# Kernel tuning notes

Measured on AMD Instinct MI355X. Metric: run time of the kernel, lower is better.

Reference implementation:

```python
import jax, jax.numpy as jnp
import numpy as np

TOP_K = 8
DILATION = 2
KERNEL = 7
W_POS = 1.0
W_NEG = 0.1
EPS = 1e-8  # torch F.cosine_similarity eps


def unfold(x, k, d):
    # nn.Unfold(kernel_size=k, padding=(k//2)*d, dilation=d) -> [B, C, k*k, H, W]
    B, C, H, W = x.shape
    p = (k // 2) * d
    xp = jnp.pad(x, ((0, 0), (0, 0), (p, p), (p, p)))
    patches = [xp[:, :, i * d:i * d + H, j * d:j * d + W]
               for i in range(k) for j in range(k)]
    return jnp.stack(patches, axis=2)


def setup_inputs() -> dict:
    key = jax.random.key(0)
    k1, k2, k3, k4 = jax.random.split(key, 4)
    return {
        "logits_trg": jax.random.normal(k1, (2, 19, 128, 128), dtype=jnp.float32),
        "logits_ema": jax.random.normal(k2, (2, 19, 64, 64), dtype=jnp.float32),
        "x_ema": jax.random.normal(k3, (2, 64, 32, 32), dtype=jnp.float32),
        "mix_masks": jax.random.uniform(k4, (2, 1, 128, 128), dtype=jnp.float32),
    }


def reference(logits_trg, logits_ema, x_ema, mix_masks):
    B, C, H, W = logits_trg.shape
    # ignore_mask_trg = F.interpolate(1 - mix_masks, (H,W), 'nearest') > 0.5 (already at (H,W))
    ignore = (1.0 - mix_masks) > 0.5  # [B,1,H,W] bool

    # logits_ema bilinear upsample to (H,W) (align_corners=False == half-pixel)
    logits_ema_up = jax.image.resize(logits_ema, (B, C, H, W), method='bilinear')
    unf_logits = unfold(logits_ema_up, KERNEL, DILATION)  # [B,C,K,H,W], K=k^2

    # get_sim_feat: nearest upsample (integer factor == torch 'nearest') then cosine sim
    f = H // x_ema.shape[2]
    feats = jnp.repeat(jnp.repeat(x_ema, f, axis=2), f, axis=3)  # [B,Cf,H,W]
    unf_feats = unfold(feats, KERNEL, DILATION)                  # [B,Cf,K,H,W]
    dot = jnp.einsum('bckhw,bchw->bkhw', unf_feats, feats)
    n_u = jnp.maximum(jnp.sqrt(jnp.sum(unf_feats * unf_feats, axis=1)), EPS)  # [B,K,H,W]
    n_c = jnp.maximum(jnp.sqrt(jnp.sum(feats * feats, axis=1)), EPS)          # [B,H,W]
    sim_feat = dot / (n_u * n_c[:, None])  # [B,K,H,W]

    # top-k over kernel window (largest top_k+1, smallest top_k)
    sim_t = jnp.moveaxis(sim_feat, 1, -1)             # [B,H,W,K]
    vmax, imax = jax.lax.top_k(sim_t, TOP_K + 1)
    vneg, imin = jax.lax.top_k(-sim_t, TOP_K)
    vmin = -vneg

    def weighted_agg(vals, idx):
        # vals/idx: [B,H,W,t] -> weighted sum of gathered logits over window -> [B,C,H,W]
        idx = jnp.moveaxis(idx, -1, 1)    # [B,t,H,W]
        vals = jnp.moveaxis(vals, -1, 1)  # [B,t,H,W]
        t = idx.shape[1]
        idxb = jnp.broadcast_to(idx[:, None], (B, C, t, H, W))
        g = jnp.take_along_axis(unf_logits, idxb, axis=2)  # [B,C,t,H,W]
        return jnp.sum(vals[:, None] * g, axis=2)

    pl_pos = jax.nn.softmax(weighted_agg(vmax, imax), axis=1)
    pl_neg = jax.nn.softmax(weighted_agg(vmin, imin), axis=1)

    def bce_with_logits(x, z):
        # -(z*log(sig(x)) + (1-z)*log(1-sig(x))) = (1-z)*x - log_sigmoid(x)
        return (1.0 - z) * x - jax.nn.log_sigmoid(x)

    m = ignore.astype(logits_trg.dtype)  # [B,1,H,W]
    denom = jnp.sum(m) * C               # mask repeated across C classes
    loss_pos = jnp.sum(bce_with_logits(logits_trg, pl_pos) * m) / denom
    loss_neg = jnp.sum(-bce_with_logits(logits_trg, pl_neg) * m) / denom
    return jnp.stack([loss_pos * W_POS, loss_neg * W_NEG])
```

## Files before the change

### kernel.cpp

```cpp
#include <hip/hip_runtime.h>
#include <math.h>

#define NB 2
#define NC 19
#define NH 128
#define NW 128
#define NCF 64
#define NHE 64
#define NHX 32
#define EPSC 1e-8f
#define NBLK 512

#define WS_PART_OFF 64

__device__ __forceinline__ int clampi(int v, int lo, int hi) {
    return v < lo ? lo : (v > hi ? hi : v);
}

__global__ __launch_bounds__(256) void pfst_main(
    const float* __restrict__ trg, const float* __restrict__ ema,
    const float* __restrict__ xe,  const float* __restrict__ mix,
    float* __restrict__ part)
{
    __shared__ float se[NC * 321];
    __shared__ float sx[NCF * 85];
    __shared__ float scn3[3 * 84];
    __shared__ float red[4][3];

    int tid = threadIdx.x;
    int l = tid & 3;
    int lc = l & 1;
    bool posH = (l < 2);
    int q = tid >> 2;
    int p0 = blockIdx.x * 64;
    int b = p0 >> 14;
    int h = (p0 >> 7) & 127;
    int w0 = p0 & 127;
    int w = w0 + q;

    int ey0 = (h - 7) >> 1, ex0 = (w0 - 7) >> 1;
    int by0 = (h - 6) >> 2, bx0 = (w0 - 6) >> 2;

    float xreg[21];
    {
        const float* Xb = xe + b * (NCF * NHX * NHX);
        #pragma unroll
        for (int r = 0; r < 21; r++) {
            int idx = tid + r * 256;
            int ch = idx / 84; int rr = idx - ch * 84;
            int a = rr / 21;   int d = rr - a * 21;
            int gy = clampi(by0 + a, 0, 31), gx = clampi(bx0 + d, 0, 31);
            xreg[r] = Xb[ch * (NHX * NHX) + gy * 32 + gx];
        }
    }
    float ereg[24];
    {
        const float* Eb = ema + b * NC * (NHE * NHE);
        #pragma unroll
        for (int r = 0; r < 24; r++) {
            int idx = tid + r * 256;
            if (idx < NC * 320) {
                int c = idx / 320; int rr = idx - c * 320;
                int rw = rr / 40;  int x = rr - rw * 40;
                int gy = clampi(ey0 + rw, 0, 63), gx = clampi(ex0 + x, 0, 63);
                ereg[r] = Eb[c * (NHE * NHE) + gy * 64 + gx];
            } else ereg[r] = 0.f;
        }
    }
    #pragma unroll
    for (int r = 0; r < 21; r++) {
        int idx = tid + r * 256;
        int ch = idx / 84; int rr = idx - ch * 84;
        sx[ch * 85 + rr] = xreg[r];
    }
    __syncthreads();

    if (tid < 252) {
        int cell = tid % 84;
        int chunk = tid / 84;
        int ch0 = chunk * 21;
        int nch = (chunk == 2) ? 22 : 21;
        float s = 0.f;
        #pragma unroll
        for (int cc = 0; cc < 22; cc++) {
            if (cc < nch) {
                float v = sx[(ch0 + cc) * 85 + cell];
                s = fmaf(v, v, s);
            }
        }
        scn3[chunk * 84 + cell] = s;
    }
    __syncthreads();

    float mval = mix[(b << 14) + (h << 7) + w];
    bool active = mval < 0.5f;
    float lp = 0.f, ln = 0.f;
    float cm = (active && l == 0) ? 1.f : 0.f;

    float tx[10];
    float vsel[9]; int isel[9];

    if (active) {
        const float* Tb = trg + b * NC * (NH * NW) + (h << 7) + w;
        #pragma unroll
        for (int jc = 0; jc < 10; jc++) {
            int c = lc + 2 * jc;
            tx[jc] = (c < NC) ? Tb[c * (NH * NW)] : 0.f;
        }

        int bx = (w - 6) >> 2;
        int trow[4], tcol[4];
        #pragma unroll
        for (int a = 0; a < 4; a++) trow[a] = clampi(by0 + a, 0, 31) - by0;
        #pragma unroll
        for (int d = 0; d < 4; d++) tcol[d] = clampi(bx + d, 0, 31) - bx0;
        int coffT = ((h >> 2) - by0) * 21 + ((w >> 2) - bx0);

        float dotc[16];
        #pragma unroll
        for (int e = 0; e < 16; e++) dotc[e] = 0.f;

        #pragma unroll 4
        for (int cc = 0; cc < 16; cc++) {
            const float* Sx = sx + (l * 16 + cc) * 85;
            float cv = Sx[coffT];
            #pragma unroll
            for (int a = 0; a < 4; a++) {
                int rb = trow[a] * 21;
                #pragma unroll
                for (int d = 0; d < 4; d++)
                    dotc[a * 4 + d] = fmaf(Sx[rb + tcol[d]], cv, dotc[a * 4 + d]);
            }
        }
        #pragma unroll
        for (int e = 0; e < 16; e++) {
            dotc[e] += __shfl_xor(dotc[e], 1); dotc[e] += __shfl_xor(dotc[e], 2);
        }

        float cn_c = (scn3[coffT] + scn3[84 + coffT]) + scn3[168 + coffT];
        float nc2 = 1.f / fmaxf(sqrtf(cn_c), EPSC);
        float scell[16];
        #pragma unroll
        for (int a = 0; a < 4; a++) {
            #pragma unroll
            for (int d = 0; d < 4; d++) {
                int x = trow[a] * 21 + tcol[d];
                float cn_u = (scn3[x] + scn3[84 + x]) + scn3[168 + x];
                float nu = fmaxf(sqrtf(cn_u), EPSC);
                scell[a * 4 + d] = dotc[a * 4 + d] * nc2 / nu;
            }
        }

        const int QA[7] = {0, 0, 1, 1, 2, 2, 3};
        const int QB[7] = {0, 1, 1, 2, 2, 3, 3};
        bool ry = (h & 3) >= 2, rx = (w & 3) >= 2;

        float sims[49];
        #pragma unroll
        for (int i = 0; i < 7; i++) {
            int py = h + 2 * i - 6;
            bool vy = (unsigned)py < 128u;
            float srow[4];
            #pragma unroll
            for (int d = 0; d < 4; d++)
                srow[d] = ry ? scell[QA[i] * 4 + d] : scell[QB[i] * 4 + d];
            #pragma unroll
            for (int j = 0; j < 7; j++) {
                int px = w + 2 * j - 6;
                bool vx = (unsigned)px < 128u;
                float v = rx ? srow[QA[j]] : srow[QB[j]];
                float sv = (vy && vx) ? v : 0.f;
                sims[i * 7 + j] = posH ? sv : -sv;
            }
        }

        float hv[25];
        #pragma unroll
        for (int kk = 0; kk < 25; kk++) {
            float aa = sims[kk];
            float bb = (kk < 24) ? sims[25 + kk] : -3.4e38f;
            hv[kk] = lc ? bb : aa;
        }
        int k0 = lc * 25;
        {
            unsigned mymask = 0u;
            #pragma unroll
            for (int t = 0; t < 9; t++) {
                float best = -3.4e38f; int bkk = 30;
                #pragma unroll
                for (int kk = 0; kk < 25; kk++) {
                    if (!((mymask >> kk) & 1u) && hv[kk] > best) { best = hv[kk]; bkk = kk; }
                }
                int bi = k0 + bkk;
                float ov = __shfl_xor(best, 1);
                int   oi = __shfl_xor(bi, 1);
                if (ov > best || (ov == best && oi < bi)) { best = ov; bi = oi; }
                vsel[t] = best; isel[t] = bi;
                int rel = bi - k0;
                if ((unsigned)rel < 25u) mymask |= 1u << rel;
            }
        }
    }

    #pragma unroll
    for (int r = 0; r < 24; r++) {
        int idx = tid + r * 256;
        if (idx < NC * 320) {
            int c = idx / 320; int rr = idx - c * 320;
            se[c * 321 + rr] = ereg[r];
        }
    }
    __syncthreads();

    if (active) {
        float av[10];
        #pragma unroll
        for (int jc = 0; jc < 10; jc++) av[jc] = 0.f;

        #pragma unroll
        for (int t = 0; t < 9; t++) {
            if (posH || t < 8) {
                int k = isel[t];
                float val = posH ? vsel[t] : -vsel[t];
                int i = (k * 586) >> 12; int j = k - 7 * i;
                int py = h + 2 * i - 6, px = w + 2 * j - 6;
                if ((unsigned)py < 128u && (unsigned)px < 128u) {
                    int iy0 = (py - 1) >> 1; float ty = (py & 1) ? 0.25f : 0.75f;
                    int ix0 = (px - 1) >> 1; float txx = (px & 1) ? 0.25f : 0.75f;
                    int y0 = clampi(iy0, 0, 63), y1 = clampi(iy0 + 1, 0, 63);
                    int x0 = clampi(ix0, 0, 63), x1 = clampi(ix0 + 1, 0, 63);
                    float w00 = (1.f - ty) * (1.f - txx), w01 = (1.f - ty) * txx;
                    float w10 = ty * (1.f - txx),         w11 = ty * txx;
                    int o00 = (y0 - ey0) * 40 + (x0 - ex0), o01 = (y0 - ey0) * 40 + (x1 - ex0);
                    int o10 = (y1 - ey0) * 40 + (x0 - ex0), o11 = (y1 - ey0) * 40 + (x1 - ex0);
                    #pragma unroll
                    for (int jc = 0; jc < 10; jc++) {
                        int c = lc + 2 * jc;
                        if (c < NC) {
                            const float* Sc = se + c * 321;
                            float g = w00 * Sc[o00] + w01 * Sc[o01]
                                    + w10 * Sc[o10] + w11 * Sc[o11];
                            av[jc] = fmaf(val, g, av[jc]);
                        }
                    }
                }
            }
        }

        float m = -3.4e38f;
        #pragma unroll
        for (int jc = 0; jc < 10; jc++) {
            int c = lc + 2 * jc;
            if (c < NC) m = fmaxf(m, av[jc]);
        }
        m = fmaxf(m, __shfl_xor(m, 1));

        float Z = 0.f, S = 0.f, Bs = 0.f;
        #pragma unroll
        for (int jc = 0; jc < 10; jc++) {
            int c = lc + 2 * jc;
            if (c < NC) {
                float x = tx[jc];
                float e = expf(av[jc] - m); Z += e; S += e * x;
                float ls = fminf(x, 0.f) - log1pf(expf(-fabsf(x)));
                Bs += x - ls;
            }
        }
        Z += __shfl_xor(Z, 1); S += __shfl_xor(S, 1); Bs += __shfl_xor(Bs, 1);

        float res = posH ? (Bs - S / Z) : (S / Z - Bs);
        float oth = __shfl_xor(res, 2);
        lp = (l == 0) ? res : 0.f;
        ln = (l == 0) ? oth : 0.f;
    }

    #pragma unroll
    for (int off = 32; off > 0; off >>= 1) {
        lp += __shfl_down(lp, off);
        ln += __shfl_down(ln, off);
        cm += __shfl_down(cm, off);
    }
    int wid = tid >> 6;
    if ((tid & 63) == 0) { red[wid][0] = lp; red[wid][1] = ln; red[wid][2] = cm; }
    __syncthreads();
    if (tid == 0) {
        float* pb = part + 3 * blockIdx.x;
        pb[0] = red[0][0] + red[1][0] + red[2][0] + red[3][0];
        pb[1] = red[0][1] + red[1][1] + red[2][1] + red[3][1];
        pb[2] = red[0][2] + red[1][2] + red[2][2] + red[3][2];
    }
}

__global__ __launch_bounds__(256) void pfst_final(const float* __restrict__ part,
                                                  float* __restrict__ out) {
    int t = threadIdx.x;
    float lp = part[3 * t + 0] + part[3 * (t + 256) + 0];
    float ln = part[3 * t + 1] + part[3 * (t + 256) + 1];
    float cm = part[3 * t + 2] + part[3 * (t + 256) + 2];
    #pragma unroll
    for (int off = 32; off > 0; off >>= 1) {
        lp += __shfl_down(lp, off);
        ln += __shfl_down(ln, off);
        cm += __shfl_down(cm, off);
    }
    __shared__ float red[4][3];
    int wid = t >> 6;
    if ((t & 63) == 0) { red[wid][0] = lp; red[wid][1] = ln; red[wid][2] = cm; }
    __syncthreads();
    if (t == 0) {
        float a0 = red[0][0] + red[1][0] + red[2][0] + red[3][0];
        float a1 = red[0][1] + red[1][1] + red[2][1] + red[3][1];
        float a2 = red[0][2] + red[1][2] + red[2][2] + red[3][2];
        float denom = a2 * (float)NC;
        out[0] = a0 / denom;
        out[1] = a1 / denom * 0.1f;
    }
}

extern "C" void kernel_launch(void* const* d_in, const int* in_sizes, int n_in,
                              void* d_out, int out_size, void* d_ws, size_t ws_size,
                              hipStream_t stream) {
    const float* trg = (const float*)d_in[0];
    const float* ema = (const float*)d_in[1];
    const float* xe  = (const float*)d_in[2];
    const float* mix = (const float*)d_in[3];
    float* part = (float*)((char*)d_ws + WS_PART_OFF);
    float* out  = (float*)d_out;

    hipLaunchKernelGGL(pfst_main, dim3(NBLK), dim3(256), 0, stream,
                       trg, ema, xe, mix, part);
    hipLaunchKernelGGL(pfst_final, dim3(1), dim3(256), 0, stream, part, out);
}
```

Before: 33.83 us.

## Share similarity and top-k work across paired pixels in 8-lane groups

```diff
diff --git a/kernel.cpp b/kernel.cpp
--- a/kernel.cpp
+++ b/kernel.cpp
@@ -29,6 +29,7 @@
 
     int tid = threadIdx.x;
     int l = tid & 3;
+    int u = tid & 7;
     int lc = l & 1;
     bool posH = (l < 2);
     int q = tid >> 2;
@@ -94,6 +95,10 @@
 
     float mval = mix[(b << 14) + (h << 7) + w];
     bool active = mval < 0.5f;
+    float af = active ? 1.f : 0.f;
+    af += __shfl_xor(af, 4);
+    bool apair = (af > 0.f);
+
     float lp = 0.f, ln = 0.f;
     float cm = (active && l == 0) ? 1.f : 0.f;
 
@@ -107,7 +112,9 @@
             int c = lc + 2 * jc;
             tx[jc] = (c < NC) ? Tb[c * (NH * NW)] : 0.f;
         }
-
+    }
+
+    if (apair) {
         int bx = (w - 6) >> 2;
         int trow[4], tcol[4];
         #pragma unroll
@@ -120,9 +127,9 @@
         #pragma unroll
         for (int e = 0; e < 16; e++) dotc[e] = 0.f;
 
-        #pragma unroll 4
-        for (int cc = 0; cc < 16; cc++) {
-            const float* Sx = sx + (l * 16 + cc) * 85;
+        #pragma unroll
+        for (int cc = 0; cc < 8; cc++) {
+            const float* Sx = sx + (u * 8 + cc) * 85;
             float cv = Sx[coffT];
             #pragma unroll
             for (int a = 0; a < 4; a++) {
@@ -134,7 +141,9 @@
         }
         #pragma unroll
         for (int e = 0; e < 16; e++) {
-            dotc[e] += __shfl_xor(dotc[e], 1); dotc[e] += __shfl_xor(dotc[e], 2);
+            dotc[e] += __shfl_xor(dotc[e], 1);
+            dotc[e] += __shfl_xor(dotc[e], 2);
+            dotc[e] += __shfl_xor(dotc[e], 4);
         }
 
         float cn_c = (scn3[coffT] + scn3[84 + coffT]) + scn3[168 + coffT];
@@ -154,6 +163,7 @@
         const int QA[7] = {0, 0, 1, 1, 2, 2, 3};
         const int QB[7] = {0, 1, 1, 2, 2, 3, 3};
         bool ry = (h & 3) >= 2, rx = (w & 3) >= 2;
+        bool posScan = (u < 4);
 
         float sims[49];
         #pragma unroll
@@ -170,35 +180,53 @@
                 bool vx = (unsigned)px < 128u;
                 float v = rx ? srow[QA[j]] : srow[QB[j]];
                 float sv = (vy && vx) ? v : 0.f;
-                sims[i * 7 + j] = posH ? sv : -sv;
-            }
-        }
-
-        float hv[25];
-        #pragma unroll
-        for (int kk = 0; kk < 25; kk++) {
-            float aa = sims[kk];
-            float bb = (kk < 24) ? sims[25 + kk] : -3.4e38f;
-            hv[kk] = lc ? bb : aa;
-        }
-        int k0 = lc * 25;
+                sims[i * 7 + j] = posScan ? sv : -sv;
+            }
+        }
+
+        int s4 = u & 3;
+        float hv[13];
+        #pragma unroll
+        for (int kk = 0; kk < 13; kk++) {
+            float v0 = (kk < 12) ? sims[kk]      : -3.4e38f;
+            float v1 = (kk < 12) ? sims[12 + kk] : -3.4e38f;
+            float v2 = (kk < 12) ? sims[24 + kk] : -3.4e38f;
+            float v3 = sims[36 + kk];
+            float lo = (s4 & 1) ? v1 : v0;
+            float hi = (s4 & 1) ? v3 : v2;
+            hv[kk] = (s4 & 2) ? hi : lo;
+        }
+        int k0 = s4 * 12;
+        int nown = (s4 == 3) ? 13 : 12;
         {
             unsigned mymask = 0u;
             #pragma unroll
             for (int t = 0; t < 9; t++) {
-                float best = -3.4e38f; int bkk = 30;
+                float best = -3.4e38f; int bkk = 20;
                 #pragma unroll
-                for (int kk = 0; kk < 25; kk++) {
+                for (int kk = 0; kk < 13; kk++) {
                     if (!((mymask >> kk) & 1u) && hv[kk] > best) { best = hv[kk]; bkk = kk; }
                 }
                 int bi = k0 + bkk;
-                float ov = __shfl_xor(best, 1);
-                int   oi = __shfl_xor(bi, 1);
-                if (ov > best || (ov == best && oi < bi)) { best = ov; bi = oi; }
+                #pragma unroll
+                for (int st = 1; st <= 2; st <<= 1) {
+                    float ov = __shfl_xor(best, st);
+                    int   oi = __shfl_xor(bi, st);
+                    if (ov > best || (ov == best && oi < bi)) { best = ov; bi = oi; }
+                }
                 vsel[t] = best; isel[t] = bi;
                 int rel = bi - k0;
-                if ((unsigned)rel < 25u) mymask |= 1u << rel;
-            }
+                if ((unsigned)rel < (unsigned)nown) mymask |= 1u << rel;
+            }
+        }
+
+        bool useOwn = ((u < 4) == (l < 2));
+        #pragma unroll
+        for (int t = 0; t < 9; t++) {
+            float ov = __shfl_xor(vsel[t], 4);
+            int   oi = __shfl_xor(isel[t], 4);
+            vsel[t] = useOwn ? vsel[t] : ov;
+            isel[t] = useOwn ? isel[t] : oi;
         }
     }
 
```

New measurement: 31.24 us. -7.7%, faster.
